# Kernel optimization log

Hardware: AMD Instinct MI355X
Metric: run time of the kernel (lower is better)

The kernel has to match this reference:

```python
import jax, jax.numpy as jnp
import numpy as np

_K = 256  # d_model // 8


def setup_inputs() -> dict:
    key = jax.random.key(0)
    ks = jax.random.split(key, 7)
    B, T, D = 4, 4096, 2048
    x = jax.random.normal(ks[0], (B, T, D), jnp.float32)
    ema_mean = 0.1 * jax.random.normal(ks[1], (D,), jnp.float32)
    # ensure positive variance: ema_sq - ema_mean^2 in [0.5, 1.5]
    ema_sq = ema_mean ** 2 + 0.5 + jax.random.uniform(ks[2], (D,), jnp.float32)
    ema_out = jax.random.normal(ks[3], (D,), jnp.float32)
    log_tau = 0.1 * jax.random.normal(ks[4], (), jnp.float32)
    log_sigma_raw = 0.1 * jax.random.normal(ks[5], (), jnp.float32)
    log_w_raw = 0.1 * jax.random.normal(ks[6], (), jnp.float32)
    return {
        "x": x,
        "ema_mean": ema_mean,
        "ema_sq": ema_sq,
        "ema_out": ema_out,
        "log_tau": log_tau,
        "log_sigma_raw": log_sigma_raw,
        "log_w_raw": log_w_raw,
    }


def reference(x, ema_mean, ema_sq, ema_out, log_tau, log_sigma_raw, log_w_raw):
    tau = jnp.exp(log_tau)
    sigma = jax.nn.softplus(log_sigma_raw) + 0.01
    w = jax.nn.softplus(log_w_raw)

    out = jax.nn.gelu(x, approximate=False)  # F.gelu default = exact erf

    # z-score against EMA stats
    std = jnp.sqrt(jnp.clip(ema_sq - ema_mean ** 2, 1e-6, None))
    z = (x - ema_mean) / std

    # topk |z| over channel dim, gather z, mean of |z_topk|
    _, idx = jax.lax.top_k(jnp.abs(z), _K)          # idx: [B,T,K]
    z_topk = jnp.take_along_axis(z, idx, axis=-1)
    topk_mean = jnp.mean(jnp.abs(z_topk), axis=-1, keepdims=True)  # [B,T,1]
    surp = jnp.tanh(sigma * topk_mean)

    # cosine similarity of gelu output against EMA output direction
    ema_u = ema_out / (jnp.linalg.norm(ema_out) + 1e-8)
    out_n = out / jnp.maximum(
        jnp.linalg.norm(out, axis=-1, keepdims=True), 1e-12
    )  # F.normalize eps
    cos_out = jnp.sum(out_n * ema_u, axis=-1, keepdims=True)  # [B,T,1]

    gate = jnp.exp(-tau * cos_out) * (1.0 + w * surp)
    return out * gate
```

## Files before the change

### kernel.cpp

```cpp
#include <hip/hip_runtime.h>
#include <math.h>

#define D      2048
#define KSEL   256
#define NT     256
#define NBINS  256
#define INV_BIN 0.03125f

__device__ __forceinline__ float fast_gelu(float x) {
    float x2 = x * x;
    float t  = fmaf(x2, -0.0713548162f, -1.5957691216f);
    float e  = __expf(x * t);
    return x * __builtin_amdgcn_rcpf(1.0f + e);
}

__global__ __launch_bounds__(NT) void fused_kernel(
    const float* __restrict__ x,
    const float* __restrict__ ema_mean,
    const float* __restrict__ ema_sq,
    const float* __restrict__ ema_out,
    const float* __restrict__ p_log_tau,
    const float* __restrict__ p_log_sigma,
    const float* __restrict__ p_log_w,
    float* __restrict__ out)
{
    __shared__ int   hist[NBINS];
    __shared__ int   wsum[4];
    __shared__ float red[4][4];
    __shared__ int   bsel_sh, krem_sh;
    __shared__ float sc_sh[3];

    const int tid = threadIdx.x;
    const size_t rowoff = (size_t)blockIdx.x * D;
    const float* __restrict__ xr = x + rowoff;

    hist[tid] = 0;
    if (tid == 0) {
        float lt = p_log_tau[0], ls = p_log_sigma[0], lw = p_log_w[0];
        sc_sh[0] = __expf(lt);
        sc_sh[1] = __logf(1.0f + __expf(ls)) + 0.01f;
        sc_sh[2] = __logf(1.0f + __expf(lw));
    }

    float4 xa = ((const float4*)xr)[tid];
    float4 xb = ((const float4*)xr)[tid + NT];
    float4 ma = ((const float4*)ema_mean)[tid];
    float4 mb = ((const float4*)ema_mean)[tid + NT];
    float4 qa = ((const float4*)ema_sq)[tid];
    float4 qb = ((const float4*)ema_sq)[tid + NT];
    float4 ea = ((const float4*)ema_out)[tid];
    float4 eb = ((const float4*)ema_out)[tid + NT];

    float xv[8] = {xa.x,xa.y,xa.z,xa.w, xb.x,xb.y,xb.z,xb.w};
    float mv[8] = {ma.x,ma.y,ma.z,ma.w, mb.x,mb.y,mb.z,mb.w};
    float qv[8] = {qa.x,qa.y,qa.z,qa.w, qb.x,qb.y,qb.z,qb.w};
    float ev[8] = {ea.x,ea.y,ea.z,ea.w, eb.x,eb.y,eb.z,eb.w};

    float g[8], av[8];
    float dot = 0.f, nrm = 0.f, ss = 0.f;
#pragma unroll
    for (int j = 0; j < 8; ++j) {
        float m = mv[j];
        float v = fmaxf(fmaf(-m, m, qv[j]), 1e-6f);
        float z = (xv[j] - m) * __builtin_amdgcn_rsqf(v);
        av[j] = fabsf(z);
        float gg = fast_gelu(xv[j]);
        g[j] = gg;
        dot = fmaf(gg, ev[j], dot);
        nrm = fmaf(gg, gg, nrm);
        ss  = fmaf(ev[j], ev[j], ss);
    }

    __syncthreads();
#pragma unroll
    for (int j = 0; j < 8; ++j) {
        int b = (int)fminf(av[j] * 32.0f, 255.0f);
        atomicAdd(&hist[b], 1);
    }
    __syncthreads();

    {
        int bin = (NBINS - 1) - tid;
        int h = hist[bin];
        int p = h;
#pragma unroll
        for (int o = 1; o < 64; o <<= 1) {
            int t = __shfl_up(p, o, 64);
            if ((tid & 63) >= o) p += t;
        }
        if ((tid & 63) == 63) wsum[tid >> 6] = p;
        __syncthreads();
        int off = 0;
        for (int wv = 0; wv < (tid >> 6); ++wv) off += wsum[wv];
        int suf_incl = p + off;
        int suf_excl = suf_incl - h;
        if (suf_excl < KSEL && suf_incl >= KSEL) {
            bsel_sh = bin;
            krem_sh = KSEL - suf_excl;
        }
    }
    __syncthreads();

    const int   bsel = bsel_sh;
    const float hi   = (float)(bsel + 1) * INV_BIN;
    const float mid  = ((float)bsel + 0.5f) * INV_BIN;

    float s = 0.f;
#pragma unroll
    for (int j = 0; j < 8; ++j) {
        s += (av[j] >= hi) ? av[j] : 0.f;
    }

#pragma unroll
    for (int o = 32; o > 0; o >>= 1) {
        dot += __shfl_down(dot, o, 64);
        nrm += __shfl_down(nrm, o, 64);
        ss  += __shfl_down(ss,  o, 64);
        s   += __shfl_down(s,   o, 64);
    }
    const int wave = tid >> 6;
    if ((tid & 63) == 0) {
        red[wave][0] = dot; red[wave][1] = nrm;
        red[wave][2] = ss;  red[wave][3] = s;
    }
    __syncthreads();
    dot = red[0][0] + red[1][0] + red[2][0] + red[3][0];
    nrm = red[0][1] + red[1][1] + red[2][1] + red[3][1];
    ss  = red[0][2] + red[1][2] + red[2][2] + red[3][2];
    s   = red[0][3] + red[1][3] + red[2][3] + red[3][3];

    const float tau = sc_sh[0], sigma = sc_sh[1], w = sc_sh[2];
    const float topk_mean = (s + (float)krem_sh * mid) * (1.0f / (float)KSEL);
    const float cosv = dot / ((sqrtf(ss) + 1e-8f) * fmaxf(sqrtf(nrm), 1e-12f));
    const float yt = sigma * topk_mean;
    const float et = __expf(-2.0f * yt);
    const float th = (1.0f - et) * __builtin_amdgcn_rcpf(1.0f + et);
    const float gate = __expf(-tau * cosv) * fmaf(w, th, 1.0f);

    float4 oa, ob;
    oa.x = g[0]*gate; oa.y = g[1]*gate; oa.z = g[2]*gate; oa.w = g[3]*gate;
    ob.x = g[4]*gate; ob.y = g[5]*gate; ob.z = g[6]*gate; ob.w = g[7]*gate;
    float* outr = out + rowoff;
    ((float4*)outr)[tid]      = oa;
    ((float4*)outr)[tid + NT] = ob;
}

extern "C" void kernel_launch(void* const* d_in, const int* in_sizes, int n_in,
                              void* d_out, int out_size, void* d_ws, size_t ws_size,
                              hipStream_t stream) {
    (void)in_sizes; (void)n_in; (void)out_size; (void)d_ws; (void)ws_size;
    const float* x         = (const float*)d_in[0];
    const float* ema_mean  = (const float*)d_in[1];
    const float* ema_sq    = (const float*)d_in[2];
    const float* ema_out   = (const float*)d_in[3];
    const float* log_tau   = (const float*)d_in[4];
    const float* log_sigma = (const float*)d_in[5];
    const float* log_w     = (const float*)d_in[6];
    float* out = (float*)d_out;

    const int rows = 4 * 4096;
    fused_kernel<<<rows, NT, 0, stream>>>(x, ema_mean, ema_sq, ema_out,
                                          log_tau, log_sigma, log_w, out);
}
```

Baseline: 55.70 us.

## Precompute per-channel z-score scale/offset and normalized EMA direction in prep kernel

Adds a single-block prep kernel that folds mean/variance into a per-channel scale and offset (pre-multiplied by the bin width), normalizes ema_out, and computes the scalar parameters once. The row kernel then does one FMA per element for the histogram key and drops the redundant ema_out norm reduction. Output stores become nontemporal. The cost is an extra small kernel launch and workspace traffic, while the per-row memory reads stay similar.

```diff
diff --git a/kernel.cpp b/kernel.cpp
--- a/kernel.cpp
+++ b/kernel.cpp
@@ -5,7 +5,8 @@
 #define KSEL   256
 #define NT     256
 #define NBINS  256
-#define INV_BIN 0.03125f
+
+typedef float vfloat4 __attribute__((ext_vector_type(4)));
 
 __device__ __forceinline__ float fast_gelu(float x) {
     float x2 = x * x;
@@ -14,67 +15,95 @@
     return x * __builtin_amdgcn_rcpf(1.0f + e);
 }
 
-__global__ __launch_bounds__(NT) void fused_kernel(
-    const float* __restrict__ x,
+__global__ __launch_bounds__(NT) void prep_kernel(
     const float* __restrict__ ema_mean,
     const float* __restrict__ ema_sq,
     const float* __restrict__ ema_out,
     const float* __restrict__ p_log_tau,
     const float* __restrict__ p_log_sigma,
     const float* __restrict__ p_log_w,
+    float* __restrict__ ws)
+{
+    __shared__ float red[4];
+    const int tid = threadIdx.x;
+    float ss = 0.f;
+#pragma unroll
+    for (int k = 0; k < D / NT; ++k) {
+        int i = tid + k * NT;
+        float m = ema_mean[i];
+        float v = fmaxf(fmaf(-m, m, ema_sq[i]), 1e-6f);
+        float inv = 32.0f * __builtin_amdgcn_rsqf(v);
+        ws[i]     = inv;
+        ws[D + i] = -m * inv;
+        float e = ema_out[i];
+        ss = fmaf(e, e, ss);
+    }
+#pragma unroll
+    for (int o = 32; o > 0; o >>= 1) ss += __shfl_down(ss, o, 64);
+    if ((tid & 63) == 0) red[tid >> 6] = ss;
+    __syncthreads();
+    float inv_nrm = 1.0f / (sqrtf(red[0] + red[1] + red[2] + red[3]) + 1e-8f);
+#pragma unroll
+    for (int k = 0; k < D / NT; ++k) {
+        int i = tid + k * NT;
+        ws[2 * D + i] = ema_out[i] * inv_nrm;
+    }
+    if (tid == 0) {
+        ws[3 * D + 0] = __expf(p_log_tau[0]);
+        ws[3 * D + 1] = __logf(1.0f + __expf(p_log_sigma[0])) + 0.01f;
+        ws[3 * D + 2] = __logf(1.0f + __expf(p_log_w[0]));
+    }
+}
+
+__global__ __launch_bounds__(NT) void row_kernel(
+    const float* __restrict__ x,
+    const float* __restrict__ ws,
     float* __restrict__ out)
 {
     __shared__ int   hist[NBINS];
     __shared__ int   wsum[4];
-    __shared__ float red[4][4];
+    __shared__ float red[4][3];
     __shared__ int   bsel_sh, krem_sh;
-    __shared__ float sc_sh[3];
 
     const int tid = threadIdx.x;
     const size_t rowoff = (size_t)blockIdx.x * D;
     const float* __restrict__ xr = x + rowoff;
 
     hist[tid] = 0;
-    if (tid == 0) {
-        float lt = p_log_tau[0], ls = p_log_sigma[0], lw = p_log_w[0];
-        sc_sh[0] = __expf(lt);
-        sc_sh[1] = __logf(1.0f + __expf(ls)) + 0.01f;
-        sc_sh[2] = __logf(1.0f + __expf(lw));
-    }
+
+    const float tau   = ws[3 * D + 0];
+    const float sigma = ws[3 * D + 1];
+    const float w     = ws[3 * D + 2];
 
     float4 xa = ((const float4*)xr)[tid];
     float4 xb = ((const float4*)xr)[tid + NT];
-    float4 ma = ((const float4*)ema_mean)[tid];
-    float4 mb = ((const float4*)ema_mean)[tid + NT];
-    float4 qa = ((const float4*)ema_sq)[tid];
-    float4 qb = ((const float4*)ema_sq)[tid + NT];
-    float4 ea = ((const float4*)ema_out)[tid];
-    float4 eb = ((const float4*)ema_out)[tid + NT];
+    float4 aa = ((const float4*)ws)[tid];
+    float4 ab = ((const float4*)ws)[tid + NT];
+    float4 ba = ((const float4*)(ws + D))[tid];
+    float4 bb = ((const float4*)(ws + D))[tid + NT];
+    float4 ua = ((const float4*)(ws + 2 * D))[tid];
+    float4 ub = ((const float4*)(ws + 2 * D))[tid + NT];
 
     float xv[8] = {xa.x,xa.y,xa.z,xa.w, xb.x,xb.y,xb.z,xb.w};
-    float mv[8] = {ma.x,ma.y,ma.z,ma.w, mb.x,mb.y,mb.z,mb.w};
-    float qv[8] = {qa.x,qa.y,qa.z,qa.w, qb.x,qb.y,qb.z,qb.w};
-    float ev[8] = {ea.x,ea.y,ea.z,ea.w, eb.x,eb.y,eb.z,eb.w};
+    float avv[8] = {aa.x,aa.y,aa.z,aa.w, ab.x,ab.y,ab.z,ab.w};
+    float bvv[8] = {ba.x,ba.y,ba.z,ba.w, bb.x,bb.y,bb.z,bb.w};
+    float uv[8] = {ua.x,ua.y,ua.z,ua.w, ub.x,ub.y,ub.z,ub.w};
 
     float g[8], av[8];
-    float dot = 0.f, nrm = 0.f, ss = 0.f;
+    float dot = 0.f, nrm = 0.f;
 #pragma unroll
     for (int j = 0; j < 8; ++j) {
-        float m = mv[j];
-        float v = fmaxf(fmaf(-m, m, qv[j]), 1e-6f);
-        float z = (xv[j] - m) * __builtin_amdgcn_rsqf(v);
-        av[j] = fabsf(z);
+        av[j] = fabsf(fmaf(xv[j], avv[j], bvv[j]));
         float gg = fast_gelu(xv[j]);
         g[j] = gg;
-        dot = fmaf(gg, ev[j], dot);
+        dot = fmaf(gg, uv[j], dot);
         nrm = fmaf(gg, gg, nrm);
-        ss  = fmaf(ev[j], ev[j], ss);
     }
 
     __syncthreads();
 #pragma unroll
     for (int j = 0; j < 8; ++j) {
-        int b = (int)fminf(av[j] * 32.0f, 255.0f);
+        int b = (int)fminf(av[j], 255.0f);
         atomicAdd(&hist[b], 1);
     }
     __syncthreads();
@@ -102,8 +131,8 @@
     __syncthreads();
 
     const int   bsel = bsel_sh;
-    const float hi   = (float)(bsel + 1) * INV_BIN;
-    const float mid  = ((float)bsel + 0.5f) * INV_BIN;
+    const float hi  = (bsel == NBINS - 1) ? __builtin_inff() : (float)(bsel + 1);
+    const float mid = (float)bsel + 0.5f;
 
     float s = 0.f;
 #pragma unroll
@@ -115,40 +144,36 @@
     for (int o = 32; o > 0; o >>= 1) {
         dot += __shfl_down(dot, o, 64);
         nrm += __shfl_down(nrm, o, 64);
-        ss  += __shfl_down(ss,  o, 64);
         s   += __shfl_down(s,   o, 64);
     }
     const int wave = tid >> 6;
     if ((tid & 63) == 0) {
-        red[wave][0] = dot; red[wave][1] = nrm;
-        red[wave][2] = ss;  red[wave][3] = s;
+        red[wave][0] = dot; red[wave][1] = nrm; red[wave][2] = s;
     }
     __syncthreads();
     dot = red[0][0] + red[1][0] + red[2][0] + red[3][0];
     nrm = red[0][1] + red[1][1] + red[2][1] + red[3][1];
-    ss  = red[0][2] + red[1][2] + red[2][2] + red[3][2];
-    s   = red[0][3] + red[1][3] + red[2][3] + red[3][3];
+    s   = red[0][2] + red[1][2] + red[2][2] + red[3][2];
 
-    const float tau = sc_sh[0], sigma = sc_sh[1], w = sc_sh[2];
-    const float topk_mean = (s + (float)krem_sh * mid) * (1.0f / (float)KSEL);
-    const float cosv = dot / ((sqrtf(ss) + 1e-8f) * fmaxf(sqrtf(nrm), 1e-12f));
+    const float topk_mean = (s + (float)krem_sh * mid) * (1.0f / (32.0f * KSEL));
+    const float cosv = dot * __builtin_amdgcn_rsqf(fmaxf(nrm, 1e-24f));
     const float yt = sigma * topk_mean;
     const float et = __expf(-2.0f * yt);
     const float th = (1.0f - et) * __builtin_amdgcn_rcpf(1.0f + et);
     const float gate = __expf(-tau * cosv) * fmaf(w, th, 1.0f);
 
-    float4 oa, ob;
+    vfloat4 oa, ob;
     oa.x = g[0]*gate; oa.y = g[1]*gate; oa.z = g[2]*gate; oa.w = g[3]*gate;
     ob.x = g[4]*gate; ob.y = g[5]*gate; ob.z = g[6]*gate; ob.w = g[7]*gate;
-    float* outr = out + rowoff;
-    ((float4*)outr)[tid]      = oa;
-    ((float4*)outr)[tid + NT] = ob;
+    vfloat4* outr = (vfloat4*)(out + rowoff);
+    __builtin_nontemporal_store(oa, outr + tid);
+    __builtin_nontemporal_store(ob, outr + tid + NT);
 }
 
 extern "C" void kernel_launch(void* const* d_in, const int* in_sizes, int n_in,
                               void* d_out, int out_size, void* d_ws, size_t ws_size,
                               hipStream_t stream) {
-    (void)in_sizes; (void)n_in; (void)out_size; (void)d_ws; (void)ws_size;
+    (void)in_sizes; (void)n_in; (void)out_size; (void)ws_size;
     const float* x         = (const float*)d_in[0];
     const float* ema_mean  = (const float*)d_in[1];
     const float* ema_sq    = (const float*)d_in[2];
@@ -157,8 +182,10 @@
     const float* log_sigma = (const float*)d_in[5];
     const float* log_w     = (const float*)d_in[6];
     float* out = (float*)d_out;
+    float* ws  = (float*)d_ws;
 
+    prep_kernel<<<1, NT, 0, stream>>>(ema_mean, ema_sq, ema_out,
+                                      log_tau, log_sigma, log_w, ws);
     const int rows = 4 * 4096;
-    fused_kernel<<<rows, NT, 0, stream>>>(x, ema_mean, ema_sq, ema_out,
-                                          log_tau, log_sigma, log_w, out);
+    row_kernel<<<rows, NT, 0, stream>>>(x, ws, out);
 }
```

Result: faster. 51.71 us (-7.2%).
